# Performance work log

Measured on AMD Instinct MI355X. Metric: run time of the kernel, lower is better.

The kernel has to match this reference:

```python
import jax, jax.numpy as jnp
import numpy as np

B, N, D = 4, 4096, 128

def setup_inputs() -> dict:
    key = jax.random.key(0)
    k1, k2 = jax.random.split(key)
    x = jax.random.normal(k1, (B, N, D), dtype=jnp.float32)
    a = jax.random.normal(k2, (2 * D, 1), dtype=jnp.float32)
    return {"x": x, "a": a}

def reference(x, a):
    # matmul(cat([x_i, x_j], -1), a) == x_i @ a1 + x_j @ a2, so avoid the
    # O(B*N*N*2D) concat: compute two O(B*N) projections and broadcast-add.
    a1 = a[:D, 0]   # [D]
    a2 = a[D:, 0]   # [D]
    s_i = x @ a1    # [B, N]  (row / source term)
    s_j = x @ a2    # [B, N]  (col / target term)
    e = s_i[:, :, None] + s_j[:, None, :]          # [B, N, N]
    e = jnp.where(e > 0, e, 0.2 * e)               # leaky_relu(0.2)
    attention = jax.nn.softmax(e, axis=-1)         # row softmax
    return attention[..., None]                    # [B, N, N, 1]
```

## Files before the change

kernel.cpp:

```cpp
#include <hip/hip_runtime.h>

#define BB 4
#define NN 4096
#define DD 128
#define RB 8

__global__ __launch_bounds__(256) void score_kernel(const float* __restrict__ x,
                                                    const float* __restrict__ a,
                                                    float* __restrict__ si,
                                                    float2* __restrict__ e12) {
    int wave = threadIdx.x >> 6;
    int lane = threadIdx.x & 63;
    int row  = blockIdx.x * 4 + wave;
    const float* xr = x + (size_t)row * DD;
    float x0 = xr[lane];
    float x1 = xr[lane + 64];
    float d1 = x0 * a[lane]      + x1 * a[lane + 64];
    float d2 = x0 * a[DD + lane] + x1 * a[DD + lane + 64];
    #pragma unroll
    for (int off = 1; off < 64; off <<= 1) {
        d1 += __shfl_xor(d1, off, 64);
        d2 += __shfl_xor(d2, off, 64);
    }
    if (lane == 0) {
        si[row] = d1;
        e12[row] = make_float2(__expf(d2), __expf(0.2f * d2));
    }
}

__global__ __launch_bounds__(256) void softmax_kernel(const float* __restrict__ si_g,
                                                      const float2* __restrict__ e12_g,
                                                      float* __restrict__ out) {
    __shared__ float red[4];

    const int b    = blockIdx.x >> 9;
    const int i0   = (blockIdx.x & 511) * RB;
    const int wave = threadIdx.x >> 6;
    const int lane = threadIdx.x & 63;

    const float* eb = (const float*)(e12_g + b * NN);
    float4 ev[32];
    float emax = 0.f;
    #pragma unroll
    for (int g = 0; g < 16; ++g) {
        const float* p = eb + (size_t)(g * 256 + lane * 4) * 2;
        ev[2 * g]     = *reinterpret_cast<const float4*>(p);
        ev[2 * g + 1] = *reinterpret_cast<const float4*>(p + 4);
        emax = fmaxf(emax, fmaxf(ev[2 * g].x,     ev[2 * g].z));
        emax = fmaxf(emax, fmaxf(ev[2 * g + 1].x, ev[2 * g + 1].z));
    }
    #pragma unroll
    for (int off = 1; off < 64; off <<= 1)
        emax = fmaxf(emax, __shfl_xor(emax, off, 64));
    if (lane == 0) red[wave] = emax;
    __syncthreads();
    const float Emax = fmaxf(fmaxf(red[0], red[1]), fmaxf(red[2], red[3]));
    const float mj = __logf(Emax);

    #pragma unroll
    for (int r = 0; r < RB / 4; ++r) {
        const int i = i0 + wave * (RB / 4) + r;
        const float sival = si_g[b * NN + i];
        const float c = sival + mj;
        const float m = c > 0.f ? c : 0.2f * c;
        const float T  = __expf(-sival);
        const float A1 = __expf(sival - m);
        const float A2 = __expf(0.2f * sival - m);

        float lsum = 0.f;
        #pragma unroll
        for (int g = 0; g < 16; ++g) {
            float4 e0 = ev[2 * g], e1 = ev[2 * g + 1];
            float p0 = (e0.x > T) ? A1 * e0.x : A2 * e0.y;
            float p1 = (e0.z > T) ? A1 * e0.z : A2 * e0.w;
            float p2 = (e1.x > T) ? A1 * e1.x : A2 * e1.y;
            float p3 = (e1.z > T) ? A1 * e1.z : A2 * e1.w;
            lsum += (p0 + p1) + (p2 + p3);
        }
        #pragma unroll
        for (int off = 1; off < 64; off <<= 1)
            lsum += __shfl_xor(lsum, off, 64);
        const float inv = 1.f / lsum;
        const float B1 = A1 * inv;
        const float B2 = A2 * inv;

        float* orow = out + (size_t)(b * NN + i) * NN;
        #pragma unroll
        for (int g = 0; g < 16; ++g) {
            float4 e0 = ev[2 * g], e1 = ev[2 * g + 1];
            float4 v;
            v.x = (e0.x > T) ? B1 * e0.x : B2 * e0.y;
            v.y = (e0.z > T) ? B1 * e0.z : B2 * e0.w;
            v.z = (e1.x > T) ? B1 * e1.x : B2 * e1.y;
            v.w = (e1.z > T) ? B1 * e1.z : B2 * e1.w;
            *reinterpret_cast<float4*>(orow + g * 256 + lane * 4) = v;
        }
    }
}

extern "C" void kernel_launch(void* const* d_in, const int* in_sizes, int n_in,
                              void* d_out, int out_size, void* d_ws, size_t ws_size,
                              hipStream_t stream) {
    const float* x = (const float*)d_in[0];
    const float* a = (const float*)d_in[1];
    float* out = (float*)d_out;
    float* si = (float*)d_ws;
    float2* e12 = (float2*)(si + BB * NN);

    score_kernel<<<(BB * NN) / 4, 256, 0, stream>>>(x, a, si, e12);
    softmax_kernel<<<(BB * NN) / RB, 256, 0, stream>>>(si, e12, out);
}
```

Baseline: 64.78 us.

## Stage column exponentials in LDS as split arrays and use max-based leaky select

Measured after the change: 87.81 us. +35.6%, slower.

```diff
diff --git a/kernel.cpp b/kernel.cpp
--- a/kernel.cpp
+++ b/kernel.cpp
@@ -8,7 +8,8 @@
 __global__ __launch_bounds__(256) void score_kernel(const float* __restrict__ x,
                                                     const float* __restrict__ a,
                                                     float* __restrict__ si,
-                                                    float2* __restrict__ e12) {
+                                                    float* __restrict__ e1,
+                                                    float* __restrict__ e2) {
     int wave = threadIdx.x >> 6;
     int lane = threadIdx.x & 63;
     int row  = blockIdx.x * 4 + wave;
@@ -24,35 +25,41 @@
     }
     if (lane == 0) {
         si[row] = d1;
-        e12[row] = make_float2(__expf(d2), __expf(0.2f * d2));
+        e1[row] = __expf(d2);
+        e2[row] = __expf(0.2f * d2);
     }
 }
 
 __global__ __launch_bounds__(256) void softmax_kernel(const float* __restrict__ si_g,
-                                                      const float2* __restrict__ e12_g,
+                                                      const float* __restrict__ e1_g,
+                                                      const float* __restrict__ e2_g,
                                                       float* __restrict__ out) {
+    __shared__ float s_e1[NN];
+    __shared__ float s_e2[NN];
     __shared__ float red[4];
 
     const int b    = blockIdx.x >> 9;
     const int i0   = (blockIdx.x & 511) * RB;
-    const int wave = threadIdx.x >> 6;
-    const int lane = threadIdx.x & 63;
+    const int tid  = threadIdx.x;
+    const int wave = tid >> 6;
+    const int lane = tid & 63;
 
-    const float* eb = (const float*)(e12_g + b * NN);
-    float4 ev[32];
-    float emax = 0.f;
+    const float* e1b = e1_g + b * NN;
+    const float* e2b = e2_g + b * NN;
+    float lmax = 0.f;
     #pragma unroll
-    for (int g = 0; g < 16; ++g) {
-        const float* p = eb + (size_t)(g * 256 + lane * 4) * 2;
-        ev[2 * g]     = *reinterpret_cast<const float4*>(p);
-        ev[2 * g + 1] = *reinterpret_cast<const float4*>(p + 4);
-        emax = fmaxf(emax, fmaxf(ev[2 * g].x,     ev[2 * g].z));
-        emax = fmaxf(emax, fmaxf(ev[2 * g + 1].x, ev[2 * g + 1].z));
+    for (int k = 0; k < 4; ++k) {
+        const int idx = k * 1024 + tid * 4;
+        float4 v1 = *reinterpret_cast<const float4*>(e1b + idx);
+        float4 v2 = *reinterpret_cast<const float4*>(e2b + idx);
+        *reinterpret_cast<float4*>(s_e1 + idx) = v1;
+        *reinterpret_cast<float4*>(s_e2 + idx) = v2;
+        lmax = fmaxf(fmaxf(fmaxf(v1.x, v1.y), fmaxf(v1.z, v1.w)), lmax);
     }
     #pragma unroll
     for (int off = 1; off < 64; off <<= 1)
-        emax = fmaxf(emax, __shfl_xor(emax, off, 64));
-    if (lane == 0) red[wave] = emax;
+        lmax = fmaxf(lmax, __shfl_xor(lmax, off, 64));
+    if (lane == 0) red[wave] = lmax;
     __syncthreads();
     const float Emax = fmaxf(fmaxf(red[0], red[1]), fmaxf(red[2], red[3]));
     const float mj = __logf(Emax);
@@ -62,20 +69,18 @@
         const int i = i0 + wave * (RB / 4) + r;
         const float sival = si_g[b * NN + i];
         const float c = sival + mj;
-        const float m = c > 0.f ? c : 0.2f * c;
-        const float T  = __expf(-sival);
+        const float m = fmaxf(c, 0.2f * c);
         const float A1 = __expf(sival - m);
         const float A2 = __expf(0.2f * sival - m);
 
         float lsum = 0.f;
         #pragma unroll
         for (int g = 0; g < 16; ++g) {
-            float4 e0 = ev[2 * g], e1 = ev[2 * g + 1];
-            float p0 = (e0.x > T) ? A1 * e0.x : A2 * e0.y;
-            float p1 = (e0.z > T) ? A1 * e0.z : A2 * e0.w;
-            float p2 = (e1.x > T) ? A1 * e1.x : A2 * e1.y;
-            float p3 = (e1.z > T) ? A1 * e1.z : A2 * e1.w;
-            lsum += (p0 + p1) + (p2 + p3);
+            const int j = g * 256 + lane * 4;
+            float4 v1 = *reinterpret_cast<const float4*>(s_e1 + j);
+            float4 v2 = *reinterpret_cast<const float4*>(s_e2 + j);
+            lsum += fmaxf(A1 * v1.x, A2 * v2.x) + fmaxf(A1 * v1.y, A2 * v2.y)
+                  + fmaxf(A1 * v1.z, A2 * v2.z) + fmaxf(A1 * v1.w, A2 * v2.w);
         }
         #pragma unroll
         for (int off = 1; off < 64; off <<= 1)
@@ -87,13 +92,14 @@
         float* orow = out + (size_t)(b * NN + i) * NN;
         #pragma unroll
         for (int g = 0; g < 16; ++g) {
-            float4 e0 = ev[2 * g], e1 = ev[2 * g + 1];
-            float4 v;
-            v.x = (e0.x > T) ? B1 * e0.x : B2 * e0.y;
-            v.y = (e0.z > T) ? B1 * e0.z : B2 * e0.w;
-            v.z = (e1.x > T) ? B1 * e1.x : B2 * e1.y;
-            v.w = (e1.z > T) ? B1 * e1.z : B2 * e1.w;
-            *reinterpret_cast<float4*>(orow + g * 256 + lane * 4) = v;
+            const int j = g * 256 + lane * 4;
+            float4 v1 = *reinterpret_cast<const float4*>(s_e1 + j);
+            float4 v2 = *reinterpret_cast<const float4*>(s_e2 + j);
+            float4 v = make_float4(fmaxf(B1 * v1.x, B2 * v2.x),
+                                   fmaxf(B1 * v1.y, B2 * v2.y),
+                                   fmaxf(B1 * v1.z, B2 * v2.z),
+                                   fmaxf(B1 * v1.w, B2 * v2.w));
+            *reinterpret_cast<float4*>(orow + j) = v;
         }
     }
 }
@@ -105,8 +111,9 @@
     const float* a = (const float*)d_in[1];
     float* out = (float*)d_out;
     float* si = (float*)d_ws;
-    float2* e12 = (float2*)(si + BB * NN);
+    float* e1 = si + BB * NN;
+    float* e2 = e1 + BB * NN;
 
-    score_kernel<<<(BB * NN) / 4, 256, 0, stream>>>(x, a, si, e12);
-    softmax_kernel<<<(BB * NN) / RB, 256, 0, stream>>>(si, e12, out);
+    score_kernel<<<(BB * NN) / 4, 256, 0, stream>>>(x, a, si, e1, e2);
+    softmax_kernel<<<(BB * NN) / RB, 256, 0, stream>>>(si, e1, e2, out);
 }
```

## Split softmax into log-sum denominator pass and exp2 streaming write pass

Applied to the files above, without the earlier changes.

Result: no change. 63.65 us (-1.7%).

```diff
diff --git a/kernel.cpp b/kernel.cpp
--- a/kernel.cpp
+++ b/kernel.cpp
@@ -5,10 +5,15 @@
 #define DD 128
 #define RB 8
 
+typedef float vf4 __attribute__((ext_vector_type(4)));
+
+__device__ __forceinline__ float ex2(float x) { return __builtin_amdgcn_exp2f(x); }
+
 __global__ __launch_bounds__(256) void score_kernel(const float* __restrict__ x,
                                                     const float* __restrict__ a,
-                                                    float* __restrict__ si,
-                                                    float2* __restrict__ e12) {
+                                                    float* __restrict__ si_lg,
+                                                    float* __restrict__ sj_lg) {
+    const float L2E = 1.4426950408889634f;
     int wave = threadIdx.x >> 6;
     int lane = threadIdx.x & 63;
     int row  = blockIdx.x * 4 + wave;
@@ -23,77 +28,92 @@
         d2 += __shfl_xor(d2, off, 64);
     }
     if (lane == 0) {
-        si[row] = d1;
-        e12[row] = make_float2(__expf(d2), __expf(0.2f * d2));
+        si_lg[row] = d1 * L2E;
+        sj_lg[row] = d2 * L2E;
     }
 }
 
-__global__ __launch_bounds__(256) void softmax_kernel(const float* __restrict__ si_g,
-                                                      const float2* __restrict__ e12_g,
-                                                      float* __restrict__ out) {
-    __shared__ float red[4];
+__global__ __launch_bounds__(256) void denom_kernel(const float* __restrict__ si_lg,
+                                                    const float* __restrict__ sj_lg,
+                                                    float* __restrict__ Mrow) {
+    int wave_g = blockIdx.x * 4 + (threadIdx.x >> 6);
+    int lane   = threadIdx.x & 63;
+    int b      = wave_g >> 10;
+    int i0     = (wave_g & 1023) * 4;
 
+    const float* sjb = sj_lg + b * NN;
+    vf4 e1[16], e2[16];
+    float kmax = -INFINITY;
+    #pragma unroll
+    for (int g = 0; g < 16; ++g) {
+        vf4 s = *reinterpret_cast<const vf4*>(sjb + g * 256 + lane * 4);
+        kmax = fmaxf(fmaxf(fmaxf(s.x, s.y), fmaxf(s.z, s.w)), kmax);
+        e2[g].x = ex2(0.2f * s.x); e2[g].y = ex2(0.2f * s.y);
+        e2[g].z = ex2(0.2f * s.z); e2[g].w = ex2(0.2f * s.w);
+        e1[g].x = ex2(s.x); e1[g].y = ex2(s.y);
+        e1[g].z = ex2(s.z); e1[g].w = ex2(s.w);
+    }
+    #pragma unroll
+    for (int off = 1; off < 64; off <<= 1)
+        kmax = fmaxf(kmax, __shfl_xor(kmax, off, 64));
+
+    #pragma unroll
+    for (int r = 0; r < 4; ++r) {
+        const int i = i0 + r;
+        const float si = si_lg[b * NN + i];
+        const float t  = si + kmax;
+        const float mr = fmaxf(t, 0.2f * t);
+        const float A1 = ex2(si - mr);
+        const float A2 = ex2(0.2f * si - mr);
+        float sum = 0.f;
+        #pragma unroll
+        for (int g = 0; g < 16; ++g) {
+            sum += fmaxf(A1 * e1[g].x, A2 * e2[g].x)
+                 + fmaxf(A1 * e1[g].y, A2 * e2[g].y)
+                 + fmaxf(A1 * e1[g].z, A2 * e2[g].z)
+                 + fmaxf(A1 * e1[g].w, A2 * e2[g].w);
+        }
+        #pragma unroll
+        for (int off = 1; off < 64; off <<= 1)
+            sum += __shfl_xor(sum, off, 64);
+        if (lane == 0)
+            Mrow[b * NN + i] = mr + __builtin_amdgcn_logf(sum);
+    }
+}
+
+__global__ __launch_bounds__(256) void stream_kernel(const float* __restrict__ si_lg,
+                                                     const float* __restrict__ sj_lg,
+                                                     const float* __restrict__ Mrow,
+                                                     float* __restrict__ out) {
     const int b    = blockIdx.x >> 9;
     const int i0   = (blockIdx.x & 511) * RB;
     const int wave = threadIdx.x >> 6;
     const int lane = threadIdx.x & 63;
 
-    const float* eb = (const float*)(e12_g + b * NN);
-    float4 ev[32];
-    float emax = 0.f;
+    const float* sjb = sj_lg + b * NN;
+    vf4 sv[16];
     #pragma unroll
-    for (int g = 0; g < 16; ++g) {
-        const float* p = eb + (size_t)(g * 256 + lane * 4) * 2;
-        ev[2 * g]     = *reinterpret_cast<const float4*>(p);
-        ev[2 * g + 1] = *reinterpret_cast<const float4*>(p + 4);
-        emax = fmaxf(emax, fmaxf(ev[2 * g].x,     ev[2 * g].z));
-        emax = fmaxf(emax, fmaxf(ev[2 * g + 1].x, ev[2 * g + 1].z));
-    }
-    #pragma unroll
-    for (int off = 1; off < 64; off <<= 1)
-        emax = fmaxf(emax, __shfl_xor(emax, off, 64));
-    if (lane == 0) red[wave] = emax;
-    __syncthreads();
-    const float Emax = fmaxf(fmaxf(red[0], red[1]), fmaxf(red[2], red[3]));
-    const float mj = __logf(Emax);
+    for (int g = 0; g < 16; ++g)
+        sv[g] = *reinterpret_cast<const vf4*>(sjb + g * 256 + lane * 4);
 
     #pragma unroll
     for (int r = 0; r < RB / 4; ++r) {
         const int i = i0 + wave * (RB / 4) + r;
-        const float sival = si_g[b * NN + i];
-        const float c = sival + mj;
-        const float m = c > 0.f ? c : 0.2f * c;
-        const float T  = __expf(-sival);
-        const float A1 = __expf(sival - m);
-        const float A2 = __expf(0.2f * sival - m);
-
-        float lsum = 0.f;
-        #pragma unroll
-        for (int g = 0; g < 16; ++g) {
-            float4 e0 = ev[2 * g], e1 = ev[2 * g + 1];
-            float p0 = (e0.x > T) ? A1 * e0.x : A2 * e0.y;
-            float p1 = (e0.z > T) ? A1 * e0.z : A2 * e0.w;
-            float p2 = (e1.x > T) ? A1 * e1.x : A2 * e1.y;
-            float p3 = (e1.z > T) ? A1 * e1.z : A2 * e1.w;
-            lsum += (p0 + p1) + (p2 + p3);
-        }
-        #pragma unroll
-        for (int off = 1; off < 64; off <<= 1)
-            lsum += __shfl_xor(lsum, off, 64);
-        const float inv = 1.f / lsum;
-        const float B1 = A1 * inv;
-        const float B2 = A2 * inv;
+        const float si = si_lg[b * NN + i];
+        const float M  = Mrow[b * NN + i];
+        const float u  = si - M;
+        const float v  = 0.2f * si - M;
 
         float* orow = out + (size_t)(b * NN + i) * NN;
         #pragma unroll
         for (int g = 0; g < 16; ++g) {
-            float4 e0 = ev[2 * g], e1 = ev[2 * g + 1];
-            float4 v;
-            v.x = (e0.x > T) ? B1 * e0.x : B2 * e0.y;
-            v.y = (e0.z > T) ? B1 * e0.z : B2 * e0.w;
-            v.z = (e1.x > T) ? B1 * e1.x : B2 * e1.y;
-            v.w = (e1.z > T) ? B1 * e1.z : B2 * e1.w;
-            *reinterpret_cast<float4*>(orow + g * 256 + lane * 4) = v;
+            vf4 s = sv[g];
+            vf4 o;
+            o.x = ex2(fmaxf(u + s.x, fmaf(0.2f, s.x, v)));
+            o.y = ex2(fmaxf(u + s.y, fmaf(0.2f, s.y, v)));
+            o.z = ex2(fmaxf(u + s.z, fmaf(0.2f, s.z, v)));
+            o.w = ex2(fmaxf(u + s.w, fmaf(0.2f, s.w, v)));
+            *reinterpret_cast<vf4*>(orow + g * 256 + lane * 4) = o;
         }
     }
 }
@@ -104,9 +124,11 @@
     const float* x = (const float*)d_in[0];
     const float* a = (const float*)d_in[1];
     float* out = (float*)d_out;
-    float* si = (float*)d_ws;
-    float2* e12 = (float2*)(si + BB * NN);
+    float* si_lg = (float*)d_ws;
+    float* sj_lg = si_lg + BB * NN;
+    float* Mrow  = sj_lg + BB * NN;
 
-    score_kernel<<<(BB * NN) / 4, 256, 0, stream>>>(x, a, si, e12);
-    softmax_kernel<<<(BB * NN) / RB, 256, 0, stream>>>(si, e12, out);
+    score_kernel<<<(BB * NN) / 4, 256, 0, stream>>>(x, a, si_lg, sj_lg);
+    denom_kernel<<<1024, 256, 0, stream>>>(si_lg, sj_lg, Mrow);
+    stream_kernel<<<(BB * NN) / RB, 256, 0, stream>>>(si_lg, sj_lg, Mrow, out);
 }
```
